# Kernel optimization log

Measured on AMD Instinct MI355X. Metric: run time of the kernel, lower is better.

Reference implementation:

```python
import jax, jax.numpy as jnp
import numpy as np

P = 7          # corr_size (patch size)
PAD = P // 2   # displacement radius
PP = P * P     # 49 correlation channels
CHANS = [512, 1024, 512, 256, 256, 256]
HW = [64, 32, 16, 8, 4, 2]
B = 8


def _spatial_correlation(f1, f2):
    """out[b, pi*P+pj, y, x] = sum_c f1[b,c,y,x] * f2[b,c,y+pi-PAD, x+pj-PAD] (zero pad)."""
    Bb, C, H, W = f1.shape
    f2p = jnp.pad(f2, ((0, 0), (0, 0), (PAD, PAD), (PAD, PAD)))
    outs = [jnp.sum(f1 * f2p[:, :, di:di + H, dj:dj + W], axis=1)
            for di in range(P) for dj in range(P)]
    return jnp.stack(outs, axis=1)  # [B, P*P, H, W]


def _corr_lstm_cell(feat, feat_pre, h_pre, c_pre, w, b):
    corr = jax.nn.leaky_relu(_spatial_correlation(feat, feat_pre), 0.01)  # [B,49,H,W]
    lstm_in = jnp.concatenate([corr, h_pre], axis=1)                      # [B,98,H,W]
    conv = jax.lax.conv_general_dilated(
        lstm_in, w, window_strides=(1, 1), padding='SAME',
        dimension_numbers=('NCHW', 'OIHW', 'NCHW')) + b[None, :, None, None]
    cc_i, cc_f, cc_o, cc_g = jnp.split(conv, 4, axis=1)
    i = jax.nn.sigmoid(cc_i)
    f = jax.nn.sigmoid(cc_f)
    o = jax.nn.sigmoid(cc_o)
    g = jnp.tanh(cc_g)
    c_next = f * c_pre + i * g
    h_next = o * jnp.tanh(c_next)
    return h_next, c_next, corr


def setup_inputs() -> dict:
    key = jax.random.key(0)
    ks = jax.random.split(key, 6 * 6)
    d = {}
    ki = 0
    for l in range(6):
        C, S = CHANS[l], HW[l]
        d[f'x{l}'] = 0.05 * jax.random.normal(ks[ki], (B, C, S, S), jnp.float32); ki += 1
        d[f'xp{l}'] = 0.05 * jax.random.normal(ks[ki], (B, C, S, S), jnp.float32); ki += 1
        d[f'h{l}'] = 0.1 * jax.random.normal(ks[ki], (B, PP, S, S), jnp.float32); ki += 1
        d[f'c{l}'] = 0.1 * jax.random.normal(ks[ki], (B, PP, S, S), jnp.float32); ki += 1
        fan_in = 2 * PP * 9
        lim = float(np.sqrt(6.0 / (fan_in + 4 * PP * 9)))
        d[f'w{l}'] = jax.random.uniform(ks[ki], (4 * PP, 2 * PP, 3, 3), jnp.float32, -lim, lim); ki += 1
        bias = jnp.zeros((4 * PP,), jnp.float32).at[PP:2 * PP].set(1.0)  # forget-gate bias = 1
        d[f'b{l}'] = bias; ki += 1
    return d


def reference(x0, x1, x2, x3, x4, x5,
              xp0, xp1, xp2, xp3, xp4, xp5,
              h0, h1, h2, h3, h4, h5,
              c0, c1, c2, c3, c4, c5,
              w0, w1, w2, w3, w4, w5,
              b0, b1, b2, b3, b4, b5):
    xs = [x0, x1, x2, x3, x4, x5]
    xps = [xp0, xp1, xp2, xp3, xp4, xp5]
    hs = [h0, h1, h2, h3, h4, h5]
    cs = [c0, c1, c2, c3, c4, c5]
    ws = [w0, w1, w2, w3, w4, w5]
    bs = [b0, b1, b2, b3, b4, b5]
    outs = []
    for l in range(6):
        outs.append(_corr_lstm_cell(xs[l], xps[l], hs[l], cs[l], ws[l], bs[l]))
    h_next = tuple(o[0] for o in outs)
    c_next = tuple(o[1] for o in outs)
    corrs = tuple(o[2] for o in outs)
    return h_next + c_next + corrs  # flat 18-tuple
```

## Files before the change

kernel.cpp:

```cpp
#include <hip/hip_runtime.h>
#include <stdint.h>

#define DEV __device__ __forceinline__

typedef _Float16 half2_t __attribute__((ext_vector_type(2)));
typedef _Float16 half4_t __attribute__((ext_vector_type(4)));
typedef __bf16   bf16x8  __attribute__((ext_vector_type(8)));
typedef float    floatx4 __attribute__((ext_vector_type(4)));
typedef float    floatx2 __attribute__((ext_vector_type(2)));

DEV float fdot2f(half2_t a, half2_t b, float c) {
#if __has_builtin(__builtin_amdgcn_fdot2)
  return __builtin_amdgcn_fdot2(a, b, c, false);
#else
  return c + (float)a[0] * (float)b[0] + (float)a[1] * (float)b[1];
#endif
}

DEV half2_t pkh2(float a, float b) {
#if __has_builtin(__builtin_amdgcn_cvt_pkrtz)
  return __builtin_bit_cast(half2_t, __builtin_amdgcn_cvt_pkrtz(a, b));
#else
  half2_t r; r[0] = (_Float16)a; r[1] = (_Float16)b; return r;
#endif
}

DEV uint32_t f2bf(float f) {
  uint32_t u = __float_as_uint(f);
  return (u + 0x7FFFu + ((u >> 16) & 1u)) >> 16;
}

DEV void tile_barrier() {
  __builtin_amdgcn_sched_barrier(0);
  asm volatile("s_waitcnt lgkmcnt(0)" ::: "memory");
  __builtin_amdgcn_s_barrier();
  __builtin_amdgcn_sched_barrier(0);
}

struct CorrCfg {
  const float* gx[6]; const float* gxp[6];
  int wg_start[2];
  int mid_start;
  int small_start[3];
  int S[2], C[2], tiles_x[2], tiles_pb[2], cpl[2];
  int mcpl;
  int sS[3], sC[3], sNspl[3];
  long long poff[2], mpoff, spoff[3];
};

__global__ __launch_bounds__(256)
void corr_kernel(CorrCfg cfg, _Float16* __restrict__ partial)
{
  __shared__ half2_t ldsbuf[2][2][22*40] __attribute__((aligned(16)));
  const int tid = threadIdx.x;
  int wg = blockIdx.x;

  if (wg >= cfg.small_start[0]) {
    int lvl = (wg >= cfg.small_start[2]) ? 2 : (wg >= cfg.small_start[1]) ? 1 : 0;
    long long i = (long long)(wg - cfg.small_start[lvl])*256 + tid;
    const int S = cfg.sS[lvl], C = cfg.sC[lvl], SS = S*S;
    const int nsp = cfg.sNspl[lvl];
    const long long per = (long long)8*49*SS;
    if (i >= (long long)nsp*per) return;
    int sp = (int)(i / per);
    long long rem = i - (long long)sp*per;
    const int cpl = C / nsp, cbase = sp * cpl;
    const float* X  = cfg.gx[lvl+3];
    const float* XP = cfg.gxp[lvl+3];
    int xc_ = (int)(rem % S); int yc = (int)((rem/S) % S);
    int d = (int)((rem/SS) % 49); int b = (int)(rem/((long long)49*SS));
    int yy = yc + d/7 - 3, xx = xc_ + (d%7) - 3;
    float s = 0.f;
    if (yy >= 0 && yy < S && xx >= 0 && xx < S) {
      const float* xb = X  + ((size_t)b*C + cbase)*SS + (size_t)yc*S + xc_;
      const float* pb = XP + ((size_t)b*C + cbase)*SS + (size_t)yy*S + xx;
      #pragma unroll 8
      for (int c = 0; c < cpl; ++c) s += xb[(size_t)c*SS] * pb[(size_t)c*SS];
    }
    partial[cfg.spoff[lvl] + (long long)sp*per + rem] = (_Float16)s;
    return;
  }

  if (wg >= cfg.mid_start) {
    constexpr int NT = 256, MS = 16, MC = 512;
    constexpr int ROWS = 22, COLS = 22, ST = 23;
    constexpr int SLOTS = ROWS * 6 * 2;
    constexpr int PER = 2;
    int rel = wg - cfg.mid_start;
    const int cpl = cfg.mcpl;
    const int sp = rel >> 3;
    const int b = rel & 7;
    const int tx = tid & 15, ty = tid >> 4;
    const int cbase = sp * cpl;
    const size_t SS = (size_t)MS*MS;
    const float* Xb  = cfg.gx[2]  + (size_t)b*MC*SS;
    const float* XPb = cfg.gxp[2] + (size_t)b*MC*SS;
    const size_t qoff = (size_t)ty*MS + tx;

    int f_go[PER], f_base[PER], f_col0[PER], f_pr[PER];
    bool f_ok[PER], f_val[PER];
    #pragma unroll
    for (int s = 0; s < PER; ++s) {
      int i = tid + s*NT;
      bool val = (i < SLOTS);
      int ii = val ? i : 0;
      int pr = ii & 1;
      int rest = ii >> 1;
      int q = rest % 6;
      int r = rest / 6;
      int gy = r - 3;
      int gx0 = -4 + 4*q;
      bool ok = val && gy >= 0 && gy < MS && gx0 >= 0 && (gx0 + 3) < MS;
      f_val[s] = val; f_ok[s] = ok; f_pr[s] = pr;
      f_go[s] = ok ? gy*MS + gx0 : 0;
      f_col0[s] = 4*q - 1;
      f_base[s] = r*ST;
    }

    float acc[49];
    #pragma unroll
    for (int d = 0; d < 49; ++d) acc[d] = 0.f;
    floatx4 fl[PER][2];
    float xc[4], xn[4];

#define MFILL_LOAD(c0v) { \
  _Pragma("unroll") for (int s = 0; s < PER; ++s) { \
    const float* p_ = XPb + (size_t)(cbase + (c0v) + 2*f_pr[s])*SS + f_go[s]; \
    if (f_ok[s]) { fl[s][0] = *(const floatx4*)p_; fl[s][1] = *(const floatx4*)(p_ + SS); } \
    else { fl[s][0] = (floatx4)0.f; fl[s][1] = (floatx4)0.f; } } }

#define MXLOAD(dst, c0v) { \
  _Pragma("unroll") for (int c = 0; c < 4; ++c) \
    dst[c] = Xb[(size_t)(cbase + (c0v) + c)*SS + qoff]; }

#define MFILL_STORE(bbv) { \
  _Pragma("unroll") for (int s = 0; s < PER; ++s) if (f_val[s]) { \
    half2_t* plane_ = &ldsbuf[bbv][f_pr[s]][0]; \
    _Pragma("unroll") for (int j = 0; j < 4; ++j) { \
      int col_ = f_col0[s] + j; \
      if (col_ >= 0 && col_ < COLS) \
        plane_[f_base[s] + col_] = pkh2(fl[s][0][j], fl[s][1][j]); } } }

#define MCOMPUTE(bbv) { \
  _Pragma("unroll") for (int pr = 0; pr < 2; ++pr) { \
    half2_t xq = pkh2(xc[2*pr], xc[2*pr+1]); \
    _Pragma("unroll") for (int di = 0; di < 7; ++di) { \
      const half2_t* row_ = &ldsbuf[bbv][pr][(ty+di)*ST + tx]; \
      _Pragma("unroll") for (int dj = 0; dj < 7; ++dj) \
        acc[di*7+dj] = fdot2f(xq, row_[dj], acc[di*7+dj]); } } }

    const int nchunk = cpl >> 2;
    MFILL_LOAD(0); MXLOAD(xc, 0);
    MFILL_STORE(0);
    MFILL_LOAD(4); MXLOAD(xn, 4);
    tile_barrier();
    for (int k = 0; k < nchunk; ++k) {
      const int bb = k & 1;
      if (k+1 < nchunk) MFILL_STORE(bb^1);
      if (k+2 < nchunk) MFILL_LOAD((k+2)*4);
      MCOMPUTE(bb);
      #pragma unroll
      for (int c = 0; c < 4; ++c) xc[c] = xn[c];
      if (k+2 < nchunk) MXLOAD(xn, (k+2)*4);
      tile_barrier();
    }
#undef MFILL_LOAD
#undef MXLOAD
#undef MFILL_STORE
#undef MCOMPUTE

    _Float16* P = partial + cfg.mpoff + ((size_t)sp*8 + b)*49*SS + qoff;
    #pragma unroll
    for (int d = 0; d < 49; ++d) P[(size_t)d*SS] = (_Float16)acc[d];
    return;
  }

  {
    constexpr int NT = 256, TH = 16, TW = 32;
    constexpr int ROWS = TH + 6;
    constexpr int COLS = TW + 6;
    constexpr int QUADS = 10;
    constexpr int ST = TW + 8;
    constexpr int SLOTS = ROWS * QUADS * 2;
    constexpr int PER = 2;

    int lvl = (wg >= cfg.wg_start[1]) ? 1 : 0;
    wg -= cfg.wg_start[lvl];
    const float* X  = cfg.gx[lvl];
    const float* XP = cfg.gxp[lvl];
    const int S = cfg.S[lvl], C = cfg.C[lvl];
    const int txc = cfg.tiles_x[lvl], tpb = cfg.tiles_pb[lvl], cpl = cfg.cpl[lvl];
    const int per_split = 8 * tpb;
    const int sp = wg / per_split;
    const int rem = wg - sp*per_split;
    const int b = rem / tpb;
    const int t = rem - b*tpb;
    const int y0 = (t / txc) * TH, x0t = (t % txc) * TW;
    const int tx = tid & 15, ty = tid >> 4;
    const int cbase = sp * cpl;
    const size_t SS = (size_t)S*S;
    const float* Xb  = X  + (size_t)b*C*SS;
    const float* XPb = XP + (size_t)b*C*SS;
    const int py = y0 + ty, px = x0t + 2*tx;
    const size_t qoff = (size_t)py*S + px;

    int f_go[PER], f_base[PER], f_col0[PER], f_pr[PER];
    bool f_ok[PER], f_val[PER];
    #pragma unroll
    for (int s = 0; s < PER; ++s) {
      int i = tid + s*NT;
      bool val = (i < SLOTS);
      int ii = val ? i : 0;
      int pr = ii & 1;
      int rest = ii >> 1;
      int q = rest % QUADS;
      int r = rest / QUADS;
      int gy = y0 + r - 3;
      int gx0 = x0t - 4 + 4*q;
      bool ok = val && gy >= 0 && gy < S && gx0 >= 0 && (gx0 + 3) < S;
      f_val[s] = val; f_ok[s] = ok; f_pr[s] = pr;
      f_go[s] = ok ? gy*S + gx0 : 0;
      f_col0[s] = 4*q - 1;
      f_base[s] = r*ST;
    }

    floatx2 acc[49];
    #pragma unroll
    for (int d = 0; d < 49; ++d) acc[d] = (floatx2)0.f;
    floatx4 fl[PER][2];
    floatx2 xc[4], xn[4];

#define FILL_LOAD(c0v) { \
  _Pragma("unroll") for (int s = 0; s < PER; ++s) { \
    const float* p_ = XPb + (size_t)(cbase + (c0v) + 2*f_pr[s])*SS + f_go[s]; \
    if (f_ok[s]) { fl[s][0] = *(const floatx4*)p_; fl[s][1] = *(const floatx4*)(p_ + SS); } \
    else { fl[s][0] = (floatx4)0.f; fl[s][1] = (floatx4)0.f; } } }

#define XLOAD(dst, c0v) { \
  _Pragma("unroll") for (int c = 0; c < 4; ++c) \
    dst[c] = *(const floatx2*)(Xb + (size_t)(cbase + (c0v) + c)*SS + qoff); }

#define FILL_STORE(bbv) { \
  _Pragma("unroll") for (int s = 0; s < PER; ++s) if (f_val[s]) { \
    half2_t* plane_ = &ldsbuf[bbv][f_pr[s]][0]; \
    _Pragma("unroll") for (int j = 0; j < 4; ++j) { \
      int col_ = f_col0[s] + j; \
      if (col_ >= 0 && col_ < COLS) \
        plane_[f_base[s] + col_] = pkh2(fl[s][0][j], fl[s][1][j]); } } }

#define COMPUTE(bbv) { \
  _Pragma("unroll") for (int pr = 0; pr < 2; ++pr) { \
    half2_t xqa = pkh2(xc[2*pr].x, xc[2*pr+1].x); \
    half2_t xqb = pkh2(xc[2*pr].y, xc[2*pr+1].y); \
    _Pragma("unroll") for (int di = 0; di < 7; ++di) { \
      const half2_t* row_ = &ldsbuf[bbv][pr][(ty+di)*ST + 2*tx]; \
      half2_t L_[8]; \
      _Pragma("unroll") for (int k = 0; k < 4; ++k) { \
        half4_t v_ = *(const half4_t*)(row_ + 2*k); \
        L_[2*k]   = __builtin_shufflevector(v_, v_, 0, 1); \
        L_[2*k+1] = __builtin_shufflevector(v_, v_, 2, 3); } \
      _Pragma("unroll") for (int dj = 0; dj < 7; ++dj) { \
        acc[di*7+dj].x = fdot2f(xqa, L_[dj],   acc[di*7+dj].x); \
        acc[di*7+dj].y = fdot2f(xqb, L_[dj+1], acc[di*7+dj].y); } } } }

    const int nchunk = cpl >> 2;
    FILL_LOAD(0); XLOAD(xc, 0);
    FILL_STORE(0);
    FILL_LOAD(4); XLOAD(xn, 4);
    tile_barrier();
    for (int k = 0; k < nchunk; ++k) {
      const int bb = k & 1;
      if (k+1 < nchunk) FILL_STORE(bb^1);
      if (k+2 < nchunk) FILL_LOAD((k+2)*4);
      COMPUTE(bb);
      #pragma unroll
      for (int c = 0; c < 4; ++c) xc[c] = xn[c];
      if (k+2 < nchunk) XLOAD(xn, (k+2)*4);
      tile_barrier();
    }
#undef FILL_LOAD
#undef XLOAD
#undef FILL_STORE
#undef COMPUTE

    _Float16* P = partial + cfg.poff[lvl] + ((size_t)sp*8 + b)*49*SS + qoff;
    #pragma unroll
    for (int d = 0; d < 49; ++d) {
      half2_t pko = pkh2(acc[d].x, acc[d].y);
      *(uint32_t*)(P + (size_t)d*SS) = *(const uint32_t*)&pko;
    }
  }
}

__global__ __launch_bounds__(256)
void pack_w_kernel(const float* __restrict__ w0, const float* __restrict__ w1,
                   const float* __restrict__ w2, const float* __restrict__ w3,
                   const float* __restrict__ w4, const float* __restrict__ w5,
                   uint16_t* __restrict__ wpack)
{
  int idx = blockIdx.x*256 + threadIdx.x;
  int lvl = idx / 258048;
  int e = idx - lvl*258048;
  const float* W = lvl==0?w0:lvl==1?w1:lvl==2?w2:lvl==3?w3:lvl==4?w4:w5;
  int j = e & 7, lane = (e >> 3) & 63, rest = e >> 9;
  int s = rest % 36, tt = rest / 36;
  int n  = tt*16 + (lane & 15);
  int ch = (s & 3)*32 + (lane >> 4)*8 + j;
  int tap = s >> 2, ky = tap/3, kx = tap - 3*ky;
  float v = 0.f;
  if (n < 196 && ch < 98) v = W[((n*98 + ch)*3 + ky)*3 + kx];
  wpack[idx] = (uint16_t)f2bf(v);
}

struct P2Cfg {
  int blk_start[7];
  int S[6], nsplit[6], pxg[6], lg[6], gpb[6];
  long long poff[6], lstm_off[6], corr_off[6];
  const float* h[6];
};
__global__ __launch_bounds__(256)
void pass2_kernel(P2Cfg cfg, const _Float16* __restrict__ partial,
                  uint32_t* __restrict__ lstm, float* __restrict__ dout)
{
  __shared__ float lds[64*99];
  int blk = blockIdx.x;
  int lvl = 0;
  while (lvl < 5 && blk >= cfg.blk_start[lvl+1]) ++lvl;
  int rel = blk - cfg.blk_start[lvl];
  const int S = cfg.S[lvl], Sp = S + 2, SS = S*S;
  const int PXG = cfg.pxg[lvl], lg = cfg.lg[lvl], gpb = cfg.gpb[lvl];
  const int b = rel / gpb, g = rel - b*gpb;
  const int pixbase = g * PXG;
  const int tid = threadIdx.x;
  const int nsp = cfg.nsplit[lvl];
  const size_t spstride = (size_t)8*49*SS;
  for (int e = tid; e < PXG*98; e += 256) {
    int pxl = e & (PXG-1);
    int ch  = e >> lg;
    int pix = pixbase + pxl;
    float v;
    if (ch < 49) {
      const _Float16* P = partial + cfg.poff[lvl] + ((size_t)b*49 + ch)*SS + pix;
      float s = 0.f;
      for (int sp = 0; sp < nsp; ++sp) s += (float)P[(size_t)sp*spstride];
      s = s < 0.f ? 0.01f*s : s;
      dout[cfg.corr_off[lvl] + ((size_t)b*49 + ch)*SS + pix] = s;
      v = s;
    } else {
      v = cfg.h[lvl][((size_t)b*49 + (ch - 49))*SS + pix];
    }
    lds[pxl*99 + ch] = v;
  }
  __syncthreads();
  uint32_t* Lb = lstm + (cfg.lstm_off[lvl] >> 1);
  for (int f = tid; f < (PXG << 6); f += 256) {
    int pxl = f >> 6, c2 = f & 63;
    int pix = pixbase + pxl;
    int y = pix / S, x = pix - y*S;
    int c0 = 2*c2, c1 = c0 + 1;
    float v0 = c0 < 98 ? lds[pxl*99 + c0] : 0.f;
    float v1 = c1 < 98 ? lds[pxl*99 + c1] : 0.f;
    Lb[((size_t)(b*Sp + y + 1)*Sp + (x + 1))*64 + c2] = f2bf(v0) | (f2bf(v1) << 16);
  }
}

struct CCfg {
  int wg_start[7];
  int S[6], tiles_x[6], tiles_pb[6], lwsh[6], mfc[6], mgrp[6];
  long long lstm_off[6], wp_off[6], conv_off[6];
};
__global__ __launch_bounds__(256)
void conv_kernel(CCfg cfg, const uint16_t* __restrict__ lstm,
                 const uint16_t* __restrict__ wpack, float* __restrict__ cout)
{
  int wg = blockIdx.x;
  int lvl = 0;
  while (lvl < 5 && wg >= cfg.wg_start[lvl+1]) ++lvl;
  wg -= cfg.wg_start[lvl];
  const int S = cfg.S[lvl], Sp = S + 2;
  const int lwsh = cfg.lwsh[lvl], msk = (1 << lwsh) - 1;
  const int tpb = cfg.tiles_pb[lvl];
  const int b = wg / tpb, t = wg - b*tpb;
  const int ty0 = (t / cfg.tiles_x[lvl]) << (6 - lwsh);
  const int tx0 = (t % cfg.tiles_x[lvl]) << lwsh;
  const int wave = threadIdx.x >> 6, lane = threadIdx.x & 63;
  const int nhalf = wave & 1, mhalf = wave >> 1;
  const int mfc = cfg.mfc[lvl];
  if (mhalf >= cfg.mgrp[lvl]) return;
  const int mi = lane & 15, q = lane >> 4;
  const int SS = S*S;
  const uint16_t* lb = lstm + cfg.lstm_off[lvl] + (size_t)b*Sp*Sp*128;
  int aoff[2];
  #pragma unroll
  for (int mf = 0; mf < 2; ++mf) {
    int p = mhalf*32 + mf*16 + mi;
    int pc = p < SS ? p : 0;
    int y = ty0 + (pc >> lwsh), xx = tx0 + (pc & msk);
    aoff[mf] = (y*Sp + xx)*128 + q*8;
  }
  const uint16_t* wb = wpack + cfg.wp_off[lvl]
                     + (size_t)(nhalf*7)*36*512 + (size_t)lane*8;
  floatx4 acc[2][7];
  #pragma unroll
  for (int mf = 0; mf < 2; ++mf)
    #pragma unroll
    for (int nt = 0; nt < 7; ++nt) acc[mf][nt] = (floatx4)0.0f;

#define CONV_LOAD(sv, AV, BV) { \
  int tap_ = (sv) >> 2, cs_ = (sv) & 3; \
  int ky_ = tap_ / 3, kx_ = tap_ - 3*ky_; \
  int ao_ = ((ky_*Sp + kx_) << 7) + (cs_ << 5); \
  _Pragma("unroll") for (int mf = 0; mf < 2; ++mf) \
    if (mf < mfc) AV[mf] = *(const bf16x8*)(lb + aoff[mf] + ao_); \
  _Pragma("unroll") for (int nt = 0; nt < 7; ++nt) \
    BV[nt] = *(const bf16x8*)(wb + (size_t)((nt)*36 + (sv))*512); }

#define CONV_MFMA(AV, BV) { \
  _Pragma("unroll") for (int nt = 0; nt < 7; ++nt) \
    _Pragma("unroll") for (int mf = 0; mf < 2; ++mf) \
      if (mf < mfc) acc[mf][nt] = __builtin_amdgcn_mfma_f32_16x16x32_bf16( \
                        AV[mf], BV[nt], acc[mf][nt], 0, 0, 0); }

  bf16x8 av0[2], bv0[7], av1[2], bv1[7];
  CONV_LOAD(0, av0, bv0);
  for (int s = 0; s < 36; s += 2) {
    CONV_LOAD(s+1, av1, bv1);
    CONV_MFMA(av0, bv0);
    if (s+2 < 36) CONV_LOAD(s+2, av0, bv0);
    CONV_MFMA(av1, bv1);
  }
#undef CONV_LOAD
#undef CONV_MFMA

  float* co = cout + cfg.conv_off[lvl] + (size_t)b*196*SS;
  #pragma unroll
  for (int mf = 0; mf < 2; ++mf) {
    if (mf < mfc) {
      #pragma unroll
      for (int nt = 0; nt < 7; ++nt) {
        const int n = nhalf*112 + nt*16 + mi;
        if (n < 196) {
          #pragma unroll
          for (int r = 0; r < 4; ++r) {
            const int p = mhalf*32 + mf*16 + q*4 + r;
            if (p < SS) {
              const int y = ty0 + (p >> lwsh), xx = tx0 + (p & msk);
              co[(size_t)n*SS + y*S + xx] = acc[mf][nt][r];
            }
          }
        }
      }
    }
  }
}

struct GCfg {
  int blk_start[7];
  int S[6];
  long long conv_off[6], h_off[6], c_off[6];
  const float* cpre[6]; const float* bias[6];
};
__global__ __launch_bounds__(256)
void gate_kernel(GCfg cfg, const float* __restrict__ convout, float* __restrict__ dout)
{
  int blk = blockIdx.x;
  int lvl = 0;
  while (lvl < 5 && blk >= cfg.blk_start[lvl+1]) ++lvl;
  long long e = (long long)(blk - cfg.blk_start[lvl])*256 + threadIdx.x;
  const int S = cfg.S[lvl];
  const int SS = S*S;
  if (e >= (long long)8*49*SS) return;
  int b = (int)(e / ((long long)49*SS));
  int r1 = (int)(e - (long long)b*49*SS);
  int ch = r1 / SS;
  int p  = r1 - ch*SS;
  const float* cv = convout + cfg.conv_off[lvl] + ((size_t)b*196 + ch)*SS + p;
  const float* bb = cfg.bias[lvl];
  float ci  = cv[0]              + bb[ch];
  float cf  = cv[(size_t)49*SS]  + bb[ch+49];
  float co_ = cv[(size_t)98*SS]  + bb[ch+98];
  float cg  = cv[(size_t)147*SS] + bb[ch+147];
  float ig = 1.f/(1.f + __expf(-ci));
  float fg = 1.f/(1.f + __expf(-cf));
  float og = 1.f/(1.f + __expf(-co_));
  float g  = 1.f - 2.f/(__expf(2.f*cg) + 1.f);
  float cp = cfg.cpre[lvl][e];
  float cn = fg*cp + ig*g;
  float hn = og * (1.f - 2.f/(__expf(2.f*cn) + 1.f));
  dout[cfg.h_off[lvl] + e] = hn;
  dout[cfg.c_off[lvl] + e] = cn;
}

extern "C" void kernel_launch(void* const* d_in, const int* in_sizes, int n_in,
                              void* d_out, int out_size, void* d_ws, size_t ws_size,
                              hipStream_t stream)
{
  const float *x[6], *xp[6], *h[6], *cpre[6], *w[6], *bias[6];
  for (int l = 0; l < 6; ++l) {
    x[l]    = (const float*)d_in[6*l + 0];
    xp[l]   = (const float*)d_in[6*l + 1];
    h[l]    = (const float*)d_in[6*l + 2];
    cpre[l] = (const float*)d_in[6*l + 3];
    w[l]    = (const float*)d_in[6*l + 4];
    bias[l] = (const float*)d_in[6*l + 5];
  }
  static const int SL[6] = {64,32,16,8,4,2};
  static const int CL[6] = {512,1024,512,256,256,256};
  int NSPL[6] = {8,16,16,1,1,1};

  long long hsz[6], lstm_off[6], conv_off[6], h_off[6], poff[6];
  long long a1 = 0, a2 = 0, a3 = 0;
  for (int l = 0; l < 6; ++l) {
    int S = SL[l], Sp = S + 2;
    hsz[l] = 8LL*49*S*S;
    lstm_off[l] = a1; a1 += 8LL*Sp*Sp*128;
    conv_off[l] = a2; a2 += 8LL*196*S*S;
    h_off[l]    = a3; a3 += hsz[l];
  }
  long long pa = 0;
  for (int l = 0; l < 6; ++l) { poff[l] = pa; pa += (long long)NSPL[l]*hsz[l]; }
  {
    long long pr_bytes = (pa*2 > a2*4 ? pa*2 : a2*4);
    long long need = a1*2 + 6LL*258048*2 + pr_bytes;
    if (need > (long long)ws_size) {
      NSPL[0] = 4; NSPL[1] = 8; NSPL[2] = 16;
      pa = 0;
      for (int l = 0; l < 6; ++l) { poff[l] = pa; pa += (long long)NSPL[l]*hsz[l]; }
    }
  }
  const long long GRP = a3;
  const long long LSTM_ELEMS = a1;

  uint16_t* lstm  = (uint16_t*)d_ws;
  uint16_t* wpack = (uint16_t*)((char*)d_ws + LSTM_ELEMS*2);
  _Float16* partial = (_Float16*)((char*)d_ws + LSTM_ELEMS*2 + 6LL*258048*2);
  float* convout  = (float*)partial;
  float* dout = (float*)d_out;

  {
    CorrCfg ccfg;
    static const int tpb2[2] = {8, 2};
    static const int txx2[2] = {2, 1};
    for (int l = 0; l < 6; ++l) { ccfg.gx[l] = x[l]; ccfg.gxp[l] = xp[l]; }
    int start = 0;
    for (int l = 0; l < 2; ++l) {
      ccfg.wg_start[l] = start;
      ccfg.S[l] = SL[l]; ccfg.C[l] = CL[l];
      ccfg.tiles_x[l] = txx2[l]; ccfg.tiles_pb[l] = tpb2[l];
      ccfg.cpl[l] = CL[l]/NSPL[l];
      ccfg.poff[l] = poff[l];
      start += NSPL[l]*8*tpb2[l];
    }
    ccfg.mid_start = start;
    ccfg.mcpl = CL[2]/NSPL[2];
    ccfg.mpoff = poff[2];
    start += NSPL[2]*8;
    for (int l = 0; l < 3; ++l) {
      ccfg.small_start[l] = start;
      ccfg.sS[l] = SL[l+3]; ccfg.sC[l] = CL[l+3];
      ccfg.sNspl[l] = NSPL[l+3];
      ccfg.spoff[l] = poff[l+3];
      start += (int)((NSPL[l+3]*hsz[l+3] + 255)/256);
    }
    corr_kernel<<<start, 256, 0, stream>>>(ccfg, partial);
  }
  (void)hipMemsetAsync(lstm, 0, (size_t)LSTM_ELEMS*2, stream);
  pack_w_kernel<<<6048, 256, 0, stream>>>(w[0],w[1],w[2],w[3],w[4],w[5], wpack);
  {
    P2Cfg p2; int start = 0;
    static const int PXGL[6] = {64,64,64,64,16,4};
    static const int LGL[6]  = {6,6,6,6,4,2};
    for (int l = 0; l < 6; ++l) {
      p2.blk_start[l] = start;
      int gpb = (SL[l]*SL[l]) / PXGL[l]; if (gpb < 1) gpb = 1;
      p2.gpb[l] = gpb;
      start += 8 * gpb;
      p2.S[l] = SL[l]; p2.nsplit[l] = NSPL[l];
      p2.pxg[l] = PXGL[l]; p2.lg[l] = LGL[l];
      p2.poff[l] = poff[l]; p2.lstm_off[l] = lstm_off[l];
      p2.corr_off[l] = 2*GRP + h_off[l];
      p2.h[l] = h[l];
    }
    p2.blk_start[6] = start;
    pass2_kernel<<<start, 256, 0, stream>>>(p2, partial, (uint32_t*)lstm, dout);
  }
  {
    CCfg cc;
    static const int ctpb[6] = {64, 16, 4, 1, 1, 1};
    static const int ctx[6]  = {4, 2, 1, 1, 1, 1};
    static const int clw[6]  = {4, 4, 4, 3, 2, 1};
    static const int cmfc[6] = {2, 2, 2, 2, 1, 1};
    static const int cmg[6]  = {2, 2, 2, 2, 1, 1};
    int start = 0;
    for (int l = 0; l < 6; ++l) {
      cc.wg_start[l] = start; start += 8*ctpb[l];
      cc.S[l] = SL[l]; cc.tiles_x[l] = ctx[l]; cc.tiles_pb[l] = ctpb[l];
      cc.lwsh[l] = clw[l]; cc.mfc[l] = cmfc[l]; cc.mgrp[l] = cmg[l];
      cc.lstm_off[l] = lstm_off[l];
      cc.wp_off[l] = 258048LL*l;
      cc.conv_off[l] = conv_off[l];
    }
    cc.wg_start[6] = start;
    conv_kernel<<<start, 256, 0, stream>>>(cc, lstm, wpack, convout);
  }
  {
    GCfg gc; int start = 0;
    for (int l = 0; l < 6; ++l) {
      gc.blk_start[l] = start;
      start += (int)((hsz[l] + 255)/256);
      gc.S[l] = SL[l];
      gc.conv_off[l] = conv_off[l];
      gc.h_off[l] = h_off[l];
      gc.c_off[l] = GRP + h_off[l];
      gc.cpre[l] = cpre[l];
      gc.bias[l] = bias[l];
    }
    gc.blk_start[6] = start;
    gate_kernel<<<start, 256, 0, stream>>>(gc, convout, dout);
  }
  (void)in_sizes; (void)n_in; (void)out_size; (void)ws_size;
}
```

Before: 501.7 us.

## Fuse LSTM gate epilogue into conv kernel and deepen correlation fill prefetch

```diff
diff --git a/kernel.cpp b/kernel.cpp
--- a/kernel.cpp
+++ b/kernel.cpp
@@ -120,10 +120,10 @@
     float acc[49];
     #pragma unroll
     for (int d = 0; d < 49; ++d) acc[d] = 0.f;
-    floatx4 fl[PER][2];
+    floatx4 flA[PER][2], flB[PER][2], flC[PER][2];
     float xc[4], xn[4];
 
-#define MFILL_LOAD(c0v) { \
+#define MFILL_LOAD(fl, c0v) { \
   _Pragma("unroll") for (int s = 0; s < PER; ++s) { \
     const float* p_ = XPb + (size_t)(cbase + (c0v) + 2*f_pr[s])*SS + f_go[s]; \
     if (f_ok[s]) { fl[s][0] = *(const floatx4*)p_; fl[s][1] = *(const floatx4*)(p_ + SS); } \
@@ -133,7 +133,7 @@
   _Pragma("unroll") for (int c = 0; c < 4; ++c) \
     dst[c] = Xb[(size_t)(cbase + (c0v) + c)*SS + qoff]; }
 
-#define MFILL_STORE(bbv) { \
+#define MFILL_STORE(bbv, fl) { \
   _Pragma("unroll") for (int s = 0; s < PER; ++s) if (f_val[s]) { \
     half2_t* plane_ = &ldsbuf[bbv][f_pr[s]][0]; \
     _Pragma("unroll") for (int j = 0; j < 4; ++j) { \
@@ -149,25 +149,42 @@
       _Pragma("unroll") for (int dj = 0; dj < 7; ++dj) \
         acc[di*7+dj] = fdot2f(xq, row_[dj], acc[di*7+dj]); } } }
 
+#define MXROT { _Pragma("unroll") for (int c = 0; c < 4; ++c) xc[c] = xn[c]; }
+
     const int nchunk = cpl >> 2;
-    MFILL_LOAD(0); MXLOAD(xc, 0);
-    MFILL_STORE(0);
-    MFILL_LOAD(4); MXLOAD(xn, 4);
+    MFILL_LOAD(flA, 0); MXLOAD(xc, 0);
+    MFILL_LOAD(flB, 4); MXLOAD(xn, 4);
+    MFILL_STORE(0, flA);
+    MFILL_LOAD(flC, 8);
     tile_barrier();
-    for (int k = 0; k < nchunk; ++k) {
-      const int bb = k & 1;
-      if (k+1 < nchunk) MFILL_STORE(bb^1);
-      if (k+2 < nchunk) MFILL_LOAD((k+2)*4);
-      MCOMPUTE(bb);
-      #pragma unroll
-      for (int c = 0; c < 4; ++c) xc[c] = xn[c];
-      if (k+2 < nchunk) MXLOAD(xn, (k+2)*4);
-      tile_barrier();
+    for (int k = 0; k < nchunk; k += 3) {
+      { const int bb = k & 1;
+        if (k+1 < nchunk) MFILL_STORE(bb^1, flB);
+        if (k+3 < nchunk) MFILL_LOAD(flA, (k+3)*4);
+        MCOMPUTE(bb);
+        MXROT;
+        if (k+2 < nchunk) MXLOAD(xn, (k+2)*4);
+        tile_barrier(); }
+      if (k+1 < nchunk) { const int bb = (k+1) & 1;
+        if (k+2 < nchunk) MFILL_STORE(bb^1, flC);
+        if (k+4 < nchunk) MFILL_LOAD(flB, (k+4)*4);
+        MCOMPUTE(bb);
+        MXROT;
+        if (k+3 < nchunk) MXLOAD(xn, (k+3)*4);
+        tile_barrier(); }
+      if (k+2 < nchunk) { const int bb = (k+2) & 1;
+        if (k+3 < nchunk) MFILL_STORE(bb^1, flA);
+        if (k+5 < nchunk) MFILL_LOAD(flC, (k+5)*4);
+        MCOMPUTE(bb);
+        MXROT;
+        if (k+4 < nchunk) MXLOAD(xn, (k+4)*4);
+        tile_barrier(); }
     }
 #undef MFILL_LOAD
 #undef MXLOAD
 #undef MFILL_STORE
 #undef MCOMPUTE
+#undef MXROT
 
     _Float16* P = partial + cfg.mpoff + ((size_t)sp*8 + b)*49*SS + qoff;
     #pragma unroll
@@ -227,10 +244,10 @@
     floatx2 acc[49];
     #pragma unroll
     for (int d = 0; d < 49; ++d) acc[d] = (floatx2)0.f;
-    floatx4 fl[PER][2];
+    floatx4 flA[PER][2], flB[PER][2], flC[PER][2];
     floatx2 xc[4], xn[4];
 
-#define FILL_LOAD(c0v) { \
+#define FILL_LOAD(fl, c0v) { \
   _Pragma("unroll") for (int s = 0; s < PER; ++s) { \
     const float* p_ = XPb + (size_t)(cbase + (c0v) + 2*f_pr[s])*SS + f_go[s]; \
     if (f_ok[s]) { fl[s][0] = *(const floatx4*)p_; fl[s][1] = *(const floatx4*)(p_ + SS); } \
@@ -240,7 +257,7 @@
   _Pragma("unroll") for (int c = 0; c < 4; ++c) \
     dst[c] = *(const floatx2*)(Xb + (size_t)(cbase + (c0v) + c)*SS + qoff); }
 
-#define FILL_STORE(bbv) { \
+#define FILL_STORE(bbv, fl) { \
   _Pragma("unroll") for (int s = 0; s < PER; ++s) if (f_val[s]) { \
     half2_t* plane_ = &ldsbuf[bbv][f_pr[s]][0]; \
     _Pragma("unroll") for (int j = 0; j < 4; ++j) { \
@@ -263,25 +280,42 @@
         acc[di*7+dj].x = fdot2f(xqa, L_[dj],   acc[di*7+dj].x); \
         acc[di*7+dj].y = fdot2f(xqb, L_[dj+1], acc[di*7+dj].y); } } } }
 
+#define XROT { _Pragma("unroll") for (int c = 0; c < 4; ++c) xc[c] = xn[c]; }
+
     const int nchunk = cpl >> 2;
-    FILL_LOAD(0); XLOAD(xc, 0);
-    FILL_STORE(0);
-    FILL_LOAD(4); XLOAD(xn, 4);
+    FILL_LOAD(flA, 0); XLOAD(xc, 0);
+    FILL_LOAD(flB, 4); XLOAD(xn, 4);
+    FILL_STORE(0, flA);
+    FILL_LOAD(flC, 8);
     tile_barrier();
-    for (int k = 0; k < nchunk; ++k) {
-      const int bb = k & 1;
-      if (k+1 < nchunk) FILL_STORE(bb^1);
-      if (k+2 < nchunk) FILL_LOAD((k+2)*4);
-      COMPUTE(bb);
-      #pragma unroll
-      for (int c = 0; c < 4; ++c) xc[c] = xn[c];
-      if (k+2 < nchunk) XLOAD(xn, (k+2)*4);
-      tile_barrier();
+    for (int k = 0; k < nchunk; k += 3) {
+      { const int bb = k & 1;
+        if (k+1 < nchunk) FILL_STORE(bb^1, flB);
+        if (k+3 < nchunk) FILL_LOAD(flA, (k+3)*4);
+        COMPUTE(bb);
+        XROT;
+        if (k+2 < nchunk) XLOAD(xn, (k+2)*4);
+        tile_barrier(); }
+      if (k+1 < nchunk) { const int bb = (k+1) & 1;
+        if (k+2 < nchunk) FILL_STORE(bb^1, flC);
+        if (k+4 < nchunk) FILL_LOAD(flB, (k+4)*4);
+        COMPUTE(bb);
+        XROT;
+        if (k+3 < nchunk) XLOAD(xn, (k+3)*4);
+        tile_barrier(); }
+      if (k+2 < nchunk) { const int bb = (k+2) & 1;
+        if (k+3 < nchunk) FILL_STORE(bb^1, flA);
+        if (k+5 < nchunk) FILL_LOAD(flC, (k+5)*4);
+        COMPUTE(bb);
+        XROT;
+        if (k+4 < nchunk) XLOAD(xn, (k+4)*4);
+        tile_barrier(); }
     }
 #undef FILL_LOAD
 #undef XLOAD
 #undef FILL_STORE
 #undef COMPUTE
+#undef XROT
 
     _Float16* P = partial + cfg.poff[lvl] + ((size_t)sp*8 + b)*49*SS + qoff;
     #pragma unroll
@@ -367,12 +401,14 @@
 struct CCfg {
   int wg_start[7];
   int S[6], tiles_x[6], tiles_pb[6], lwsh[6], mfc[6], mgrp[6];
-  long long lstm_off[6], wp_off[6], conv_off[6];
+  long long lstm_off[6], wp_off[6], h_off[6], c_off[6];
+  const float* cpre[6]; const float* bias[6];
 };
 __global__ __launch_bounds__(256)
 void conv_kernel(CCfg cfg, const uint16_t* __restrict__ lstm,
-                 const uint16_t* __restrict__ wpack, float* __restrict__ cout)
+                 const uint16_t* __restrict__ wpack, float* __restrict__ dout)
 {
+  __shared__ float gl[224*69];
   int wg = blockIdx.x;
   int lvl = 0;
   while (lvl < 5 && wg >= cfg.wg_start[lvl+1]) ++lvl;
@@ -383,28 +419,31 @@
   const int b = wg / tpb, t = wg - b*tpb;
   const int ty0 = (t / cfg.tiles_x[lvl]) << (6 - lwsh);
   const int tx0 = (t % cfg.tiles_x[lvl]) << lwsh;
-  const int wave = threadIdx.x >> 6, lane = threadIdx.x & 63;
+  const int tid = threadIdx.x;
+  const int wave = tid >> 6, lane = tid & 63;
   const int nhalf = wave & 1, mhalf = wave >> 1;
   const int mfc = cfg.mfc[lvl];
-  if (mhalf >= cfg.mgrp[lvl]) return;
+  const bool active = (mhalf < cfg.mgrp[lvl]);
   const int mi = lane & 15, q = lane >> 4;
   const int SS = S*S;
-  const uint16_t* lb = lstm + cfg.lstm_off[lvl] + (size_t)b*Sp*Sp*128;
-  int aoff[2];
-  #pragma unroll
-  for (int mf = 0; mf < 2; ++mf) {
-    int p = mhalf*32 + mf*16 + mi;
-    int pc = p < SS ? p : 0;
-    int y = ty0 + (pc >> lwsh), xx = tx0 + (pc & msk);
-    aoff[mf] = (y*Sp + xx)*128 + q*8;
-  }
-  const uint16_t* wb = wpack + cfg.wp_off[lvl]
-                     + (size_t)(nhalf*7)*36*512 + (size_t)lane*8;
-  floatx4 acc[2][7];
-  #pragma unroll
-  for (int mf = 0; mf < 2; ++mf)
-    #pragma unroll
-    for (int nt = 0; nt < 7; ++nt) acc[mf][nt] = (floatx4)0.0f;
+
+  if (active) {
+    const uint16_t* lb = lstm + cfg.lstm_off[lvl] + (size_t)b*Sp*Sp*128;
+    int aoff[2];
+    #pragma unroll
+    for (int mf = 0; mf < 2; ++mf) {
+      int p = mhalf*32 + mf*16 + mi;
+      int pc = p < SS ? p : 0;
+      int y = ty0 + (pc >> lwsh), xx = tx0 + (pc & msk);
+      aoff[mf] = (y*Sp + xx)*128 + q*8;
+    }
+    const uint16_t* wb = wpack + cfg.wp_off[lvl]
+                       + (size_t)(nhalf*7)*36*512 + (size_t)lane*8;
+    floatx4 acc[2][7];
+    #pragma unroll
+    for (int mf = 0; mf < 2; ++mf)
+      #pragma unroll
+      for (int nt = 0; nt < 7; ++nt) acc[mf][nt] = (floatx4)0.0f;
 
 #define CONV_LOAD(sv, AV, BV) { \
   int tap_ = (sv) >> 2, cs_ = (sv) & 3; \
@@ -421,74 +460,61 @@
       if (mf < mfc) acc[mf][nt] = __builtin_amdgcn_mfma_f32_16x16x32_bf16( \
                         AV[mf], BV[nt], acc[mf][nt], 0, 0, 0); }
 
-  bf16x8 av0[2], bv0[7], av1[2], bv1[7];
-  CONV_LOAD(0, av0, bv0);
-  for (int s = 0; s < 36; s += 2) {
-    CONV_LOAD(s+1, av1, bv1);
-    CONV_MFMA(av0, bv0);
-    if (s+2 < 36) CONV_LOAD(s+2, av0, bv0);
-    CONV_MFMA(av1, bv1);
-  }
+    bf16x8 av0[2], bv0[7], av1[2], bv1[7];
+    CONV_LOAD(0, av0, bv0);
+    for (int s = 0; s < 36; s += 2) {
+      CONV_LOAD(s+1, av1, bv1);
+      CONV_MFMA(av0, bv0);
+      if (s+2 < 36) CONV_LOAD(s+2, av0, bv0);
+      CONV_MFMA(av1, bv1);
+    }
 #undef CONV_LOAD
 #undef CONV_MFMA
 
-  float* co = cout + cfg.conv_off[lvl] + (size_t)b*196*SS;
-  #pragma unroll
-  for (int mf = 0; mf < 2; ++mf) {
-    if (mf < mfc) {
-      #pragma unroll
-      for (int nt = 0; nt < 7; ++nt) {
-        const int n = nhalf*112 + nt*16 + mi;
-        if (n < 196) {
-          #pragma unroll
-          for (int r = 0; r < 4; ++r) {
-            const int p = mhalf*32 + mf*16 + q*4 + r;
-            if (p < SS) {
-              const int y = ty0 + (p >> lwsh), xx = tx0 + (p & msk);
-              co[(size_t)n*SS + y*S + xx] = acc[mf][nt][r];
+    #pragma unroll
+    for (int mf = 0; mf < 2; ++mf) {
+      if (mf < mfc) {
+        #pragma unroll
+        for (int nt = 0; nt < 7; ++nt) {
+          const int n = nhalf*112 + nt*16 + mi;
+          if (n < 196) {
+            #pragma unroll
+            for (int r = 0; r < 4; ++r) {
+              const int p = mhalf*32 + mf*16 + q*4 + r;
+              gl[n*69 + p] = acc[mf][nt][r];
             }
           }
         }
       }
     }
   }
-}
-
-struct GCfg {
-  int blk_start[7];
-  int S[6];
-  long long conv_off[6], h_off[6], c_off[6];
-  const float* cpre[6]; const float* bias[6];
-};
-__global__ __launch_bounds__(256)
-void gate_kernel(GCfg cfg, const float* __restrict__ convout, float* __restrict__ dout)
-{
-  int blk = blockIdx.x;
-  int lvl = 0;
-  while (lvl < 5 && blk >= cfg.blk_start[lvl+1]) ++lvl;
-  long long e = (long long)(blk - cfg.blk_start[lvl])*256 + threadIdx.x;
-  const int S = cfg.S[lvl];
-  const int SS = S*S;
-  if (e >= (long long)8*49*SS) return;
-  int b = (int)(e / ((long long)49*SS));
-  int r1 = (int)(e - (long long)b*49*SS);
-  int ch = r1 / SS;
-  int p  = r1 - ch*SS;
-  const float* cv = convout + cfg.conv_off[lvl] + ((size_t)b*196 + ch)*SS + p;
-  const float* bb = cfg.bias[lvl];
-  float ci  = cv[0]              + bb[ch];
-  float cf  = cv[(size_t)49*SS]  + bb[ch+49];
-  float co_ = cv[(size_t)98*SS]  + bb[ch+98];
-  float cg  = cv[(size_t)147*SS] + bb[ch+147];
-  float ig = 1.f/(1.f + __expf(-ci));
-  float fg = 1.f/(1.f + __expf(-cf));
-  float og = 1.f/(1.f + __expf(-co_));
-  float g  = 1.f - 2.f/(__expf(2.f*cg) + 1.f);
-  float cp = cfg.cpre[lvl][e];
-  float cn = fg*cp + ig*g;
-  float hn = og * (1.f - 2.f/(__expf(2.f*cn) + 1.f));
-  dout[cfg.h_off[lvl] + e] = hn;
-  dout[cfg.c_off[lvl] + e] = cn;
+  __syncthreads();
+
+  const int p2 = lane;
+  const int grp = wave;
+  if (p2 < SS) {
+    const int y = ty0 + (p2 >> lwsh), xx = tx0 + (p2 & msk);
+    const int pix = y*S + xx;
+    const float* bb2 = cfg.bias[lvl];
+    const float* cp  = cfg.cpre[lvl];
+    const int ch0 = grp*13, chend = (grp == 3) ? 49 : grp*13 + 13;
+    for (int ch = ch0; ch < chend; ++ch) {
+      float ci  = gl[ch*69 + p2]        + bb2[ch];
+      float cf  = gl[(ch+49)*69 + p2]   + bb2[ch+49];
+      float co_ = gl[(ch+98)*69 + p2]   + bb2[ch+98];
+      float cg  = gl[(ch+147)*69 + p2]  + bb2[ch+147];
+      float ig = 1.f/(1.f + __expf(-ci));
+      float fg = 1.f/(1.f + __expf(-cf));
+      float og = 1.f/(1.f + __expf(-co_));
+      float g  = 1.f - 2.f/(__expf(2.f*cg) + 1.f);
+      size_t e = ((size_t)b*49 + ch)*SS + pix;
+      float cpv = cp[e];
+      float cn = fg*cpv + ig*g;
+      float hn = og * (1.f - 2.f/(__expf(2.f*cn) + 1.f));
+      dout[cfg.h_off[lvl] + e] = hn;
+      dout[cfg.c_off[lvl] + e] = cn;
+    }
+  }
 }
 
 extern "C" void kernel_launch(void* const* d_in, const int* in_sizes, int n_in,
@@ -508,20 +534,18 @@
   static const int CL[6] = {512,1024,512,256,256,256};
   int NSPL[6] = {8,16,16,1,1,1};
 
-  long long hsz[6], lstm_off[6], conv_off[6], h_off[6], poff[6];
-  long long a1 = 0, a2 = 0, a3 = 0;
+  long long hsz[6], lstm_off[6], h_off[6], poff[6];
+  long long a1 = 0, a3 = 0;
   for (int l = 0; l < 6; ++l) {
     int S = SL[l], Sp = S + 2;
     hsz[l] = 8LL*49*S*S;
     lstm_off[l] = a1; a1 += 8LL*Sp*Sp*128;
-    conv_off[l] = a2; a2 += 8LL*196*S*S;
     h_off[l]    = a3; a3 += hsz[l];
   }
   long long pa = 0;
   for (int l = 0; l < 6; ++l) { poff[l] = pa; pa += (long long)NSPL[l]*hsz[l]; }
   {
-    long long pr_bytes = (pa*2 > a2*4 ? pa*2 : a2*4);
-    long long need = a1*2 + 6LL*258048*2 + pr_bytes;
+    long long need = a1*2 + 6LL*258048*2 + pa*2;
     if (need > (long long)ws_size) {
       NSPL[0] = 4; NSPL[1] = 8; NSPL[2] = 16;
       pa = 0;
@@ -534,7 +558,6 @@
   uint16_t* lstm  = (uint16_t*)d_ws;
   uint16_t* wpack = (uint16_t*)((char*)d_ws + LSTM_ELEMS*2);
   _Float16* partial = (_Float16*)((char*)d_ws + LSTM_ELEMS*2 + 6LL*258048*2);
-  float* convout  = (float*)partial;
   float* dout = (float*)d_out;
 
   {
@@ -598,25 +621,13 @@
       cc.lwsh[l] = clw[l]; cc.mfc[l] = cmfc[l]; cc.mgrp[l] = cmg[l];
       cc.lstm_off[l] = lstm_off[l];
       cc.wp_off[l] = 258048LL*l;
-      cc.conv_off[l] = conv_off[l];
+      cc.h_off[l] = h_off[l];
+      cc.c_off[l] = GRP + h_off[l];
+      cc.cpre[l] = cpre[l];
+      cc.bias[l] = bias[l];
     }
     cc.wg_start[6] = start;
-    conv_kernel<<<start, 256, 0, stream>>>(cc, lstm, wpack, convout);
-  }
-  {
-    GCfg gc; int start = 0;
-    for (int l = 0; l < 6; ++l) {
-      gc.blk_start[l] = start;
-      start += (int)((hsz[l] + 255)/256);
-      gc.S[l] = SL[l];
-      gc.conv_off[l] = conv_off[l];
-      gc.h_off[l] = h_off[l];
-      gc.c_off[l] = GRP + h_off[l];
-      gc.cpre[l] = cpre[l];
-      gc.bias[l] = bias[l];
-    }
-    gc.blk_start[6] = start;
-    gate_kernel<<<start, 256, 0, stream>>>(gc, convout, dout);
+    conv_kernel<<<start, 256, 0, stream>>>(cc, lstm, wpack, dout);
   }
   (void)in_sizes; (void)n_in; (void)out_size; (void)ws_size;
 }
```

After: 518.0 us. 3.3% more time.
